# Performance work log

Measured on AMD Instinct MI355X. Metric: run time of the kernel, lower is better.

The kernel has to match this reference:

```python
import jax, jax.numpy as jnp
import numpy as np

B, C, T, L, H = 4, 512, 8, 512, 8


def _normalize(a, eps=1e-12):
    # F.normalize: x / max(||x||_2, eps) along last dim
    n = jnp.linalg.norm(a, axis=-1, keepdims=True)
    return a / jnp.maximum(n, eps)


def setup_inputs() -> dict:
    key = jax.random.key(0)
    ks = jax.random.split(key, 8)
    w = lambda k, shp: (jax.random.normal(k, shp, dtype=jnp.float32) * 0.02)
    return {
        "e": jax.random.normal(ks[0], (B, C, T, L), dtype=jnp.float32),
        "x": jax.random.normal(ks[1], (B, C, T, L), dtype=jnp.float32),
        "Wq": w(ks[2], (C, C)), "bq": jnp.zeros((C,), jnp.float32),
        "Wkv": w(ks[3], (2 * C, C)), "bkv": jnp.zeros((2 * C,), jnp.float32),
        "Wm": w(ks[4], (C, C)), "bm": jnp.zeros((C,), jnp.float32),
        "Wg1": w(ks[5], (C, C)), "bg1": jnp.zeros((C,), jnp.float32),
        "Wg2": w(ks[6], (H, C)), "bg2": jnp.zeros((H,), jnp.float32),
    }


def reference(e, x, Wq, bq, Wkv, bkv, Wm, bm, Wg1, bg1, Wg2, bg2):
    shortcut = x
    xp = jnp.transpose(x, (0, 2, 3, 1))  # (b,t,l,c)
    ep = jnp.transpose(e, (0, 2, 3, 1))  # (b,t,l,c)
    b, t, l, c = xp.shape
    hd = c // H

    # per-(b,t) head gating from pooled e (gate_weights1 == gate_weights in source)
    pooled = ep.mean(axis=2)  # (b,t,c)
    glog = jnp.tanh(pooled @ Wg1.T + bg1) @ Wg2.T + bg2  # (b,t,H)
    gw = jax.nn.softmax(glog, axis=-1)[..., None, None]  # (b,t,H,1,1)

    q = (ep @ Wq.T + bq).reshape(b, t, l, H, hd).transpose(0, 1, 3, 2, 4)  # (b,t,H,l,hd)
    q = _normalize(q)
    kv = (xp @ Wkv.T + bkv).reshape(b, t, l, 2 * H, hd).transpose(0, 1, 3, 2, 4)
    k, v = kv[:, :, :H], kv[:, :, H:]
    k = _normalize(k)
    v = _normalize(v) * gw  # pre-softmax value gating

    scale = jnp.float32(1.0 / np.sqrt(hd))
    att = jax.nn.softmax(jnp.einsum('bthid,bthjd->bthij', q, k) * scale, axis=-1)
    o = jnp.einsum('bthij,bthjd->bthid', att, v) * gw  # post-attention gating

    o = o.transpose(0, 1, 3, 2, 4).reshape(b, t, l, c)
    o = o @ Wm.T + bm
    return jnp.transpose(o, (0, 3, 1, 2)) + shortcut
```

## Files before the change

### kernel.cpp

```cpp
#include <hip/hip_runtime.h>
#include <math.h>

#define B_ 4
#define C_ 512
#define T_ 8
#define L_ 512
#define H_ 8
#define HD_ 64

typedef unsigned short ushort_t;
using short8 = __attribute__((ext_vector_type(8))) short;
using f4 = __attribute__((ext_vector_type(4))) float;

#define GLOAD_LDS(gp, lp)                                                      \
  __builtin_amdgcn_global_load_lds(                                            \
      (const __attribute__((address_space(1))) unsigned int*)(gp),             \
      (__attribute__((address_space(3))) unsigned int*)(lp), 16, 0, 0)

__device__ __forceinline__ unsigned pack_bf16(float a, float b) {
  union { float f; unsigned u; } ua, ub;
  ua.f = a; ub.f = b;
  unsigned ra = (ua.u + 0x7FFFu + ((ua.u >> 16) & 1u)) >> 16;
  unsigned rb = (ub.u + 0x7FFFu + ((ub.u >> 16) & 1u)) >> 16;
  return (rb << 16) | (ra & 0xFFFFu);
}
__device__ __forceinline__ ushort_t bf16_1(float a) {
  union { float f; unsigned u; } ua; ua.f = a;
  return (ushort_t)((ua.u + 0x7FFFu + ((ua.u >> 16) & 1u)) >> 16);
}


__global__ __launch_bounds__(256) void pool_kernel(const float* __restrict__ e,
                                                   float* __restrict__ pooled) {
  int wave = threadIdx.x >> 6;
  int lane = threadIdx.x & 63;
  int r = blockIdx.x * 4 + wave;
  int t = r % T_;
  int c = (r / T_) % C_;
  int b = r / (T_ * C_);
  const float* row = e + (size_t)r * L_;
  float s = 0.f;
#pragma unroll
  for (int i = 0; i < L_ / 64; ++i) s += row[lane + i * 64];
#pragma unroll
  for (int off = 32; off > 0; off >>= 1) s += __shfl_down(s, off, 64);
  if (lane == 0) pooled[(b * T_ + t) * C_ + c] = s * (1.0f / L_);
}

__global__ __launch_bounds__(256) void gate1_kernel(const float* __restrict__ pooled,
                                                    const float* __restrict__ Wg1,
                                                    const float* __restrict__ bg1,
                                                    float* __restrict__ h1) {
  int w = threadIdx.x >> 6, lane = threadIdx.x & 63;
  int row = blockIdx.x * 4 + w;
  int bt = blockIdx.y;
  const float* wr = Wg1 + (size_t)row * C_;
  const float* pr = pooled + bt * C_;
  float s = 0.f;
#pragma unroll
  for (int i = 0; i < 8; ++i) s += wr[lane + i * 64] * pr[lane + i * 64];
#pragma unroll
  for (int off = 32; off > 0; off >>= 1) s += __shfl_down(s, off, 64);
  if (lane == 0) h1[bt * C_ + row] = tanhf(s + bg1[row]);
}

__global__ __launch_bounds__(256) void gate2_kernel(const float* __restrict__ h1,
                                                    const float* __restrict__ Wg2,
                                                    const float* __restrict__ bg2,
                                                    float* __restrict__ gwp) {
  __shared__ float part[256];
  __shared__ float gl[H_];
  int bt = blockIdx.x, tid = threadIdx.x;
  int h = tid >> 5, s = tid & 31;
  const float* w2 = Wg2 + (size_t)h * C_;
  const float* hb = h1 + bt * C_;
  float p = 0.f;
  for (int c = s; c < C_; c += 32) p += w2[c] * hb[c];
  part[tid] = p;
  __syncthreads();
  if (tid < H_) {
    float a = bg2[tid];
    for (int i = 0; i < 32; ++i) a += part[tid * 32 + i];
    gl[tid] = a;
  }
  __syncthreads();
  if (tid == 0) {
    float m = -1e30f;
    for (int i = 0; i < H_; ++i) m = fmaxf(m, gl[i]);
    float sum = 0.f;
    float ex[H_];
    for (int i = 0; i < H_; ++i) { ex[i] = expf(gl[i] - m); sum += ex[i]; }
    for (int i = 0; i < H_; ++i) gwp[bt * H_ + i] = ex[i] / sum;
  }
}

__global__ __launch_bounds__(256) void cvt_kernel(const float* __restrict__ s,
                                                  ushort_t* __restrict__ d) {
  int i = (blockIdx.x * 256 + threadIdx.x) * 8;
  float4 a = *(const float4*)(s + i);
  float4 b = *(const float4*)(s + i + 4);
  uint4 o;
  o.x = pack_bf16(a.x, a.y); o.y = pack_bf16(a.z, a.w);
  o.z = pack_bf16(b.x, b.y); o.w = pack_bf16(b.z, b.w);
  *(uint4*)(d + i) = o;
}

__global__ __launch_bounds__(256) void tconv_kernel(const float* __restrict__ src,
                                                    ushort_t* __restrict__ dst) {
  __shared__ float tb[64][65];
  int tid = threadIdx.x;
  int b = blockIdx.z >> 3, t = blockIdx.z & 7;
  int c0 = blockIdx.y * 64, l0 = blockIdx.x * 64;
  const float* sp = src + (((size_t)(b * C_ + c0) * T_) + t) * L_ + l0;
  int j = tid & 63, i0 = tid >> 6;
#pragma unroll
  for (int p = 0; p < 16; ++p) {
    int i = p * 4 + i0;
    tb[i][j] = sp[(size_t)i * (T_ * L_) + j];
  }
  __syncthreads();
  int ii = (tid & 31) * 2, jj0 = tid >> 5;
  ushort_t* dp = dst + ((size_t)blockIdx.z * L_ + l0) * C_ + c0;
#pragma unroll
  for (int p = 0; p < 8; ++p) {
    int jj = p * 8 + jj0;
    *(unsigned*)(dp + (size_t)jj * C_ + ii) = pack_bf16(tb[ii][jj], tb[ii + 1][jj]);
  }
}

__global__ __launch_bounds__(256, 2) void gemm_mfma(
    const ushort_t* __restrict__ A, const ushort_t* __restrict__ BT,
    const float* __restrict__ bias, int mode,
    float* __restrict__ Out, const float* __restrict__ resid,
    ushort_t* __restrict__ Kdst, ushort_t* __restrict__ Vdst,
    const float* __restrict__ gwp, float qscale) {
  __shared__ alignas(16) ushort_t As[128 * 32];
  __shared__ alignas(16) ushort_t Bs[128 * 32];
  int tid = threadIdx.x;
  int w = tid >> 6, lane = tid & 63, l15 = lane & 15, q = lane >> 4;
  int n0 = blockIdx.x * 128, m0 = blockIdx.y * 128, bt = blockIdx.z;
  int wm = (w >> 1) * 64, wn = (w & 1) * 64;
  const ushort_t* Bbt = BT + (size_t)bt * C_ * C_;

  int c0 = w * 64 + lane, c1 = 256 + w * 64 + lane;
  const ushort_t* ag0 = A + (size_t)(m0 + (c0 >> 2)) * 512 + (c0 & 3) * 8;
  const ushort_t* ag1 = A + (size_t)(m0 + (c1 >> 2)) * 512 + (c1 & 3) * 8;
  const ushort_t* bg0 = Bbt + (size_t)(n0 + (c0 >> 2)) * 512 + (c0 & 3) * 8;
  const ushort_t* bg1 = Bbt + (size_t)(n0 + (c1 >> 2)) * 512 + (c1 & 3) * 8;
  ushort_t* la0 = As + (size_t)(w * 64) * 8;
  ushort_t* la1 = As + (size_t)(256 + w * 64) * 8;
  ushort_t* lb0 = Bs + (size_t)(w * 64) * 8;
  ushort_t* lb1 = Bs + (size_t)(256 + w * 64) * 8;

  f4 acc[4][4];
#pragma unroll
  for (int i = 0; i < 4; ++i)
#pragma unroll
    for (int j = 0; j < 4; ++j) acc[i][j] = (f4){0.f, 0.f, 0.f, 0.f};

  for (int k0 = 0; k0 < 512; k0 += 32) {
    __syncthreads();
    GLOAD_LDS(ag0 + k0, la0);
    GLOAD_LDS(ag1 + k0, la1);
    GLOAD_LDS(bg0 + k0, lb0);
    GLOAD_LDS(bg1 + k0, lb1);
    __syncthreads();
    short8 af[4], bf[4];
#pragma unroll
    for (int mt = 0; mt < 4; ++mt)
      af[mt] = *(const short8*)&As[(size_t)(wm + mt * 16 + l15) * 32 + q * 8];
#pragma unroll
    for (int nt = 0; nt < 4; ++nt)
      bf[nt] = *(const short8*)&Bs[(size_t)(wn + nt * 16 + l15) * 32 + q * 8];
#pragma unroll
    for (int mt = 0; mt < 4; ++mt)
#pragma unroll
      for (int nt = 0; nt < 4; ++nt)
        acc[mt][nt] =
            __builtin_amdgcn_mfma_f32_16x16x32_bf16(af[mt], bf[nt], acc[mt][nt], 0, 0, 0);
  }

#pragma unroll
  for (int mt = 0; mt < 4; ++mt)
#pragma unroll
    for (int r = 0; r < 4; ++r) {
      float bb = bias[m0 + wm + mt * 16 + q * 4 + r];
#pragma unroll
      for (int nt = 0; nt < 4; ++nt) acc[mt][nt][r] += bb;
    }

  if (mode == 0) {
    int b = bt >> 3, t = bt & 7;
    float* Ob = Out + (size_t)b * (C_ * T_ * L_) + (size_t)t * L_;
    const float* Rb = resid + (size_t)b * (C_ * T_ * L_) + (size_t)t * L_;
#pragma unroll
    for (int mt = 0; mt < 4; ++mt)
#pragma unroll
      for (int r = 0; r < 4; ++r) {
        size_t ro = (size_t)(m0 + wm + mt * 16 + q * 4 + r) * (T_ * L_);
#pragma unroll
        for (int nt = 0; nt < 4; ++nt) {
          int n = n0 + wn + nt * 16 + l15;
          Ob[ro + n] = acc[mt][nt][r] + Rb[ro + n];
        }
      }
    return;
  }

  float scale[4];
#pragma unroll
  for (int nt = 0; nt < 4; ++nt) {
    float s = 0.f;
#pragma unroll
    for (int mt = 0; mt < 4; ++mt)
#pragma unroll
      for (int r = 0; r < 4; ++r) s += acc[mt][nt][r] * acc[mt][nt][r];
    s += __shfl_xor(s, 16);
    s += __shfl_xor(s, 32);
    scale[nt] = s;
  }
  int hh = ((m0 + wm) >> 6) & 7;
  bool isv = (mode == 2) && (m0 + wm >= 512);
  float mult = isv ? gwp[bt * H_ + hh] : qscale;
#pragma unroll
  for (int nt = 0; nt < 4; ++nt)
    scale[nt] = mult / fmaxf(sqrtf(scale[nt]), 1e-12f);

  if (!isv) {
    ushort_t* Kb = Kdst + (size_t)(bt * H_ + hh) * 512 * 64;
#pragma unroll
    for (int nt = 0; nt < 4; ++nt) {
      int l = n0 + wn + nt * 16 + l15;
      ushort_t* rowp = Kb + (size_t)l * 64;
#pragma unroll
      for (int mt = 0; mt < 4; ++mt) {
        uint2 pk;
        pk.x = pack_bf16(acc[mt][nt][0] * scale[nt], acc[mt][nt][1] * scale[nt]);
        pk.y = pack_bf16(acc[mt][nt][2] * scale[nt], acc[mt][nt][3] * scale[nt]);
        *(uint2*)&rowp[mt * 16 + q * 4] = pk;
      }
    }
  } else {
    ushort_t* Vb = Vdst + (size_t)(bt * H_ + hh) * 64 * 512;
#pragma unroll
    for (int mt = 0; mt < 4; ++mt)
#pragma unroll
      for (int r = 0; r < 4; ++r) {
        int d = mt * 16 + q * 4 + r;
        ushort_t* rp = Vb + (size_t)d * 512 + n0 + wn;
#pragma unroll
        for (int nt = 0; nt < 4; ++nt)
          rp[nt * 16 + l15] = bf16_1(acc[mt][nt][r] * scale[nt]);
      }
  }
}

__global__ __launch_bounds__(256) void attn_kernel(
    const ushort_t* __restrict__ Qbf, const ushort_t* __restrict__ Kbf,
    const ushort_t* __restrict__ Vbf, const float* __restrict__ gwp,
    ushort_t* __restrict__ obfT) {
  __shared__ alignas(16) ushort_t Ka[64 * 64];
  __shared__ alignas(16) ushort_t Va[64 * 64];

  int tid = threadIdx.x;
  int w = tid >> 6, lane = tid & 63, l15 = lane & 15, q = lane >> 4;
  int i0 = blockIdx.x * 64, h = blockIdx.y, bt = blockIdx.z;
  int iglob = i0 + w * 16 + l15;

  const ushort_t* qrow = Qbf + ((size_t)(bt * H_ + h) * 512 + iglob) * 64;
  short8 qfrag0 = *(const short8*)&qrow[q * 8];
  short8 qfrag1 = *(const short8*)&qrow[32 + q * 8];

  const ushort_t* Kg = Kbf + (size_t)(bt * H_ + h) * 512 * 64;
  const ushort_t* Vg = Vbf + (size_t)(bt * H_ + h) * 64 * 512;

  int cA = w * 64 + lane, cB = 256 + w * 64 + lane;
  const ushort_t* kg0 = Kg + (size_t)(cA >> 3) * 64 + ((cA & 7) ^ ((cA >> 3) & 7)) * 8;
  const ushort_t* kg1 = Kg + (size_t)(cB >> 3) * 64 + ((cB & 7) ^ ((cB >> 3) & 7)) * 8;
  const ushort_t* vg0 = Vg + (size_t)(cA >> 3) * 512 + ((cA & 7) ^ ((cA >> 3) & 7)) * 8;
  const ushort_t* vg1 = Vg + (size_t)(cB >> 3) * 512 + ((cB & 7) ^ ((cB >> 3) & 7)) * 8;
  ushort_t* lk0 = Ka + (size_t)(w * 64) * 8;
  ushort_t* lk1 = Ka + (size_t)(256 + w * 64) * 8;
  ushort_t* lv0 = Va + (size_t)(w * 64) * 8;
  ushort_t* lv1 = Va + (size_t)(256 + w * 64) * 8;

  f4 acc[4];
#pragma unroll
  for (int dt = 0; dt < 4; ++dt) acc[dt] = (f4){0.f, 0.f, 0.f, 0.f};
  float mrun = -3.0e38f, lrun = 0.f;
  bool hi_half = (lane >= 32);
  int qh2 = (q & 1) * 2;

  for (int j0 = 0; j0 < 512; j0 += 64) {
    __syncthreads();
    GLOAD_LDS(kg0 + (size_t)j0 * 64, lk0);
    GLOAD_LDS(kg1 + (size_t)j0 * 64, lk1);
    GLOAD_LDS(vg0 + j0, lv0);
    GLOAD_LDS(vg1 + j0, lv1);
    __syncthreads();

    f4 sc[4];
#pragma unroll
    for (int jt = 0; jt < 4; ++jt) {
      int row = jt * 16 + l15;
      int swz = row & 7;
      short8 k0 = *(const short8*)&Ka[row * 64 + ((q ^ swz) * 8)];
      short8 k1 = *(const short8*)&Ka[row * 64 + (((4 + q) ^ swz) * 8)];
      f4 c = {0.f, 0.f, 0.f, 0.f};
      c = __builtin_amdgcn_mfma_f32_16x16x32_bf16(k0, qfrag0, c, 0, 0, 0);
      c = __builtin_amdgcn_mfma_f32_16x16x32_bf16(k1, qfrag1, c, 0, 0, 0);
      sc[jt] = c;
    }

    float tm = -3.0e38f;
#pragma unroll
    for (int jt = 0; jt < 4; ++jt)
#pragma unroll
      for (int r = 0; r < 4; ++r) tm = fmaxf(tm, sc[jt][r]);
    tm = fmaxf(tm, __shfl_xor(tm, 16));
    tm = fmaxf(tm, __shfl_xor(tm, 32));
    float mn = fmaxf(mrun, tm);
    float alpha = __expf(mrun - mn);
    mrun = mn;
    float ls = 0.f;
#pragma unroll
    for (int jt = 0; jt < 4; ++jt)
#pragma unroll
      for (int r = 0; r < 4; ++r) {
        float p = __expf(sc[jt][r] - mn);
        sc[jt][r] = p;
        ls += p;
      }
    ls += __shfl_xor(ls, 16);
    ls += __shfl_xor(ls, 32);
    lrun = lrun * alpha + ls;
#pragma unroll
    for (int dt = 0; dt < 4; ++dt) acc[dt] = acc[dt] * alpha;

    unsigned pk01[4], pk23[4];
#pragma unroll
    for (int jt = 0; jt < 4; ++jt) {
      pk01[jt] = pack_bf16(sc[jt][0], sc[jt][1]);
      pk23[jt] = pack_bf16(sc[jt][2], sc[jt][3]);
    }

#pragma unroll
    for (int ks2 = 0; ks2 < 2; ++ks2) {
      union { unsigned u[4]; short8 s; } bu;
#pragma unroll
      for (int r = 0; r < 4; ++r) {
        int src = (qh2 + (r >> 1)) * 16 + l15;
        unsigned pl = (r & 1) ? pk23[ks2 * 2] : pk01[ks2 * 2];
        unsigned ph = (r & 1) ? pk23[ks2 * 2 + 1] : pk01[ks2 * 2 + 1];
        unsigned lo = __shfl(pl, src);
        unsigned hi = __shfl(ph, src);
        bu.u[r] = hi_half ? hi : lo;
      }
      short8 bfrag = bu.s;
#pragma unroll
      for (int dt = 0; dt < 4; ++dt) {
        int row = dt * 16 + l15;
        short8 vf =
            *(const short8*)&Va[row * 64 + (((ks2 * 4 + q) ^ (row & 7)) * 8)];
        acc[dt] = __builtin_amdgcn_mfma_f32_16x16x32_bf16(vf, bfrag, acc[dt], 0, 0, 0);
      }
    }
  }

  float g = gwp[bt * H_ + h];
  float inv = g / lrun;
  ushort_t* ob = obfT + ((size_t)(bt * 512 + iglob)) * 512 + h * 64;
#pragma unroll
  for (int dt = 0; dt < 4; ++dt) {
    uint2 pk;
    pk.x = pack_bf16(acc[dt][0] * inv, acc[dt][1] * inv);
    pk.y = pack_bf16(acc[dt][2] * inv, acc[dt][3] * inv);
    *(uint2*)&ob[dt * 16 + q * 4] = pk;
  }
}

extern "C" void kernel_launch(void* const* d_in, const int* in_sizes, int n_in,
                              void* d_out, int out_size, void* d_ws, size_t ws_size,
                              hipStream_t stream) {
  const float* e   = (const float*)d_in[0];
  const float* x   = (const float*)d_in[1];
  const float* Wq  = (const float*)d_in[2];
  const float* bq  = (const float*)d_in[3];
  const float* Wkv = (const float*)d_in[4];
  const float* bkv = (const float*)d_in[5];
  const float* Wm  = (const float*)d_in[6];
  const float* bm  = (const float*)d_in[7];
  const float* Wg1 = (const float*)d_in[8];
  const float* bg1 = (const float*)d_in[9];
  const float* Wg2 = (const float*)d_in[10];
  const float* bg2 = (const float*)d_in[11];
  float* out = (float*)d_out;

  float* ws = (float*)d_ws;
  float* pooled = ws;
  float* gwp    = ws + 16384;
  float* h1buf  = ws + 16640;
  float* fb     = ws + 33024;
  ushort_t* ebfT = (ushort_t*)(fb);
  ushort_t* xbfT = (ushort_t*)(fb + 1 * 4194304);
  ushort_t* Qbf  = (ushort_t*)(fb + 2 * 4194304);
  ushort_t* Kbf  = (ushort_t*)(fb + 3 * 4194304);
  ushort_t* Vbf  = (ushort_t*)(fb + 4 * 4194304);
  ushort_t* obfT = (ushort_t*)(fb + 5 * 4194304);
  ushort_t* Wqb  = (ushort_t*)(fb + 6 * 4194304);
  ushort_t* Wkvb = Wqb + 262144;
  ushort_t* Wmb  = Wkvb + 524288;

  cvt_kernel<<<dim3(128), dim3(256), 0, stream>>>(Wq, Wqb);
  cvt_kernel<<<dim3(256), dim3(256), 0, stream>>>(Wkv, Wkvb);
  cvt_kernel<<<dim3(128), dim3(256), 0, stream>>>(Wm, Wmb);
  tconv_kernel<<<dim3(8, 8, 32), dim3(256), 0, stream>>>(e, ebfT);
  tconv_kernel<<<dim3(8, 8, 32), dim3(256), 0, stream>>>(x, xbfT);
  pool_kernel<<<dim3(B_ * C_ * T_ / 4), dim3(256), 0, stream>>>(e, pooled);
  gate1_kernel<<<dim3(128, 32), dim3(256), 0, stream>>>(pooled, Wg1, bg1, h1buf);
  gate2_kernel<<<dim3(32), dim3(256), 0, stream>>>(h1buf, Wg2, bg2, gwp);
  gemm_mfma<<<dim3(4, 4, 32), dim3(256), 0, stream>>>(
      Wqb, ebfT, bq, 1, nullptr, nullptr, Qbf, nullptr, gwp, 0.125f);
  gemm_mfma<<<dim3(4, 8, 32), dim3(256), 0, stream>>>(
      Wkvb, xbfT, bkv, 2, nullptr, nullptr, Kbf, Vbf, gwp, 1.0f);
  attn_kernel<<<dim3(8, H_, 32), dim3(256), 0, stream>>>(Qbf, Kbf, Vbf, gwp, obfT);
  gemm_mfma<<<dim3(4, 4, 32), dim3(256), 0, stream>>>(
      Wmb, obfT, bm, 0, out, x, nullptr, nullptr, gwp, 1.0f);
}
```

Before: 274.7 us.

## Fuse pooling into transpose-convert and drop online softmax max in attention

The mean-pool over L is folded into the e transpose/convert kernel through atomic adds, which removes a separate full pass over e. The attention kernel is restructured so that one 512-thread block handles all 512 queries of a (bt,h) pair. Each wave holds four query fragments and reads K/V fragments straight from global memory, with no LDS staging or barriers. The running-max rescaling is dropped on the grounds that q and k are unit-normalized, so the scaled scores are bounded and exp cannot overflow. This removes the max reduction and accumulator rescale, but it relies on that normalization bound and increases register pressure.

```diff
diff --git a/kernel.cpp b/kernel.cpp
--- a/kernel.cpp
+++ b/kernel.cpp
@@ -29,23 +29,6 @@
   return (ushort_t)((ua.u + 0x7FFFu + ((ua.u >> 16) & 1u)) >> 16);
 }
 
-
-__global__ __launch_bounds__(256) void pool_kernel(const float* __restrict__ e,
-                                                   float* __restrict__ pooled) {
-  int wave = threadIdx.x >> 6;
-  int lane = threadIdx.x & 63;
-  int r = blockIdx.x * 4 + wave;
-  int t = r % T_;
-  int c = (r / T_) % C_;
-  int b = r / (T_ * C_);
-  const float* row = e + (size_t)r * L_;
-  float s = 0.f;
-#pragma unroll
-  for (int i = 0; i < L_ / 64; ++i) s += row[lane + i * 64];
-#pragma unroll
-  for (int off = 32; off > 0; off >>= 1) s += __shfl_down(s, off, 64);
-  if (lane == 0) pooled[(b * T_ + t) * C_ + c] = s * (1.0f / L_);
-}
 
 __global__ __launch_bounds__(256) void gate1_kernel(const float* __restrict__ pooled,
                                                     const float* __restrict__ Wg1,
@@ -106,7 +89,8 @@
 }
 
 __global__ __launch_bounds__(256) void tconv_kernel(const float* __restrict__ src,
-                                                    ushort_t* __restrict__ dst) {
+                                                    ushort_t* __restrict__ dst,
+                                                    float* __restrict__ pooled) {
   __shared__ float tb[64][65];
   int tid = threadIdx.x;
   int b = blockIdx.z >> 3, t = blockIdx.z & 7;
@@ -119,6 +103,15 @@
     tb[i][j] = sp[(size_t)i * (T_ * L_) + j];
   }
   __syncthreads();
+  if (pooled) {
+    int c = tid >> 2, part = tid & 3;
+    float s = 0.f;
+#pragma unroll
+    for (int k = 0; k < 16; ++k) s += tb[c][part * 16 + k];
+    s += __shfl_down(s, 1);
+    s += __shfl_down(s, 2);
+    if (part == 0) atomicAdd(&pooled[blockIdx.z * C_ + c0 + c], s * (1.0f / L_));
+  }
   int ii = (tid & 31) * 2, jj0 = tid >> 5;
   ushort_t* dp = dst + ((size_t)blockIdx.z * L_ + l0) * C_ + c0;
 #pragma unroll
@@ -255,127 +248,113 @@
   }
 }
 
-__global__ __launch_bounds__(256) void attn_kernel(
+__global__ __launch_bounds__(512, 2) void attn_kernel(
     const ushort_t* __restrict__ Qbf, const ushort_t* __restrict__ Kbf,
     const ushort_t* __restrict__ Vbf, const float* __restrict__ gwp,
     ushort_t* __restrict__ obfT) {
-  __shared__ alignas(16) ushort_t Ka[64 * 64];
-  __shared__ alignas(16) ushort_t Va[64 * 64];
-
   int tid = threadIdx.x;
   int w = tid >> 6, lane = tid & 63, l15 = lane & 15, q = lane >> 4;
-  int i0 = blockIdx.x * 64, h = blockIdx.y, bt = blockIdx.z;
-  int iglob = i0 + w * 16 + l15;
-
-  const ushort_t* qrow = Qbf + ((size_t)(bt * H_ + h) * 512 + iglob) * 64;
-  short8 qfrag0 = *(const short8*)&qrow[q * 8];
-  short8 qfrag1 = *(const short8*)&qrow[32 + q * 8];
-
+  int h = blockIdx.x, bt = blockIdx.y;
+
+  const ushort_t* Qg = Qbf + (size_t)(bt * H_ + h) * 512 * 64;
   const ushort_t* Kg = Kbf + (size_t)(bt * H_ + h) * 512 * 64;
   const ushort_t* Vg = Vbf + (size_t)(bt * H_ + h) * 64 * 512;
 
-  int cA = w * 64 + lane, cB = 256 + w * 64 + lane;
-  const ushort_t* kg0 = Kg + (size_t)(cA >> 3) * 64 + ((cA & 7) ^ ((cA >> 3) & 7)) * 8;
-  const ushort_t* kg1 = Kg + (size_t)(cB >> 3) * 64 + ((cB & 7) ^ ((cB >> 3) & 7)) * 8;
-  const ushort_t* vg0 = Vg + (size_t)(cA >> 3) * 512 + ((cA & 7) ^ ((cA >> 3) & 7)) * 8;
-  const ushort_t* vg1 = Vg + (size_t)(cB >> 3) * 512 + ((cB & 7) ^ ((cB >> 3) & 7)) * 8;
-  ushort_t* lk0 = Ka + (size_t)(w * 64) * 8;
-  ushort_t* lk1 = Ka + (size_t)(256 + w * 64) * 8;
-  ushort_t* lv0 = Va + (size_t)(w * 64) * 8;
-  ushort_t* lv1 = Va + (size_t)(256 + w * 64) * 8;
-
-  f4 acc[4];
-#pragma unroll
-  for (int dt = 0; dt < 4; ++dt) acc[dt] = (f4){0.f, 0.f, 0.f, 0.f};
-  float mrun = -3.0e38f, lrun = 0.f;
+  short8 qf[4][2];
+#pragma unroll
+  for (int f = 0; f < 4; ++f) {
+    const ushort_t* qrow = Qg + (size_t)(w * 64 + f * 16 + l15) * 64;
+    qf[f][0] = *(const short8*)&qrow[q * 8];
+    qf[f][1] = *(const short8*)&qrow[32 + q * 8];
+  }
+
+  f4 acc[4][4];
+#pragma unroll
+  for (int f = 0; f < 4; ++f)
+#pragma unroll
+    for (int dt = 0; dt < 4; ++dt) acc[f][dt] = (f4){0.f, 0.f, 0.f, 0.f};
+  float lsum[4] = {0.f, 0.f, 0.f, 0.f};
   bool hi_half = (lane >= 32);
   int qh2 = (q & 1) * 2;
 
   for (int j0 = 0; j0 < 512; j0 += 64) {
-    __syncthreads();
-    GLOAD_LDS(kg0 + (size_t)j0 * 64, lk0);
-    GLOAD_LDS(kg1 + (size_t)j0 * 64, lk1);
-    GLOAD_LDS(vg0 + j0, lv0);
-    GLOAD_LDS(vg1 + j0, lv1);
-    __syncthreads();
-
-    f4 sc[4];
+    short8 kf[4][2], vf[2][4];
 #pragma unroll
     for (int jt = 0; jt < 4; ++jt) {
-      int row = jt * 16 + l15;
-      int swz = row & 7;
-      short8 k0 = *(const short8*)&Ka[row * 64 + ((q ^ swz) * 8)];
-      short8 k1 = *(const short8*)&Ka[row * 64 + (((4 + q) ^ swz) * 8)];
-      f4 c = {0.f, 0.f, 0.f, 0.f};
-      c = __builtin_amdgcn_mfma_f32_16x16x32_bf16(k0, qfrag0, c, 0, 0, 0);
-      c = __builtin_amdgcn_mfma_f32_16x16x32_bf16(k1, qfrag1, c, 0, 0, 0);
-      sc[jt] = c;
+      const ushort_t* krow = Kg + (size_t)(j0 + jt * 16 + l15) * 64;
+      kf[jt][0] = *(const short8*)&krow[q * 8];
+      kf[jt][1] = *(const short8*)&krow[32 + q * 8];
     }
-
-    float tm = -3.0e38f;
-#pragma unroll
-    for (int jt = 0; jt < 4; ++jt)
-#pragma unroll
-      for (int r = 0; r < 4; ++r) tm = fmaxf(tm, sc[jt][r]);
-    tm = fmaxf(tm, __shfl_xor(tm, 16));
-    tm = fmaxf(tm, __shfl_xor(tm, 32));
-    float mn = fmaxf(mrun, tm);
-    float alpha = __expf(mrun - mn);
-    mrun = mn;
-    float ls = 0.f;
-#pragma unroll
-    for (int jt = 0; jt < 4; ++jt)
-#pragma unroll
-      for (int r = 0; r < 4; ++r) {
-        float p = __expf(sc[jt][r] - mn);
-        sc[jt][r] = p;
-        ls += p;
-      }
+#pragma unroll
+    for (int ks2 = 0; ks2 < 2; ++ks2)
+#pragma unroll
+      for (int dt = 0; dt < 4; ++dt)
+        vf[ks2][dt] = *(const short8*)(Vg + (size_t)(dt * 16 + l15) * 512 + j0 +
+                                       ks2 * 32 + q * 8);
+
+#pragma unroll
+    for (int f = 0; f < 4; ++f) {
+      f4 sc[4];
+#pragma unroll
+      for (int jt = 0; jt < 4; ++jt) {
+        f4 c = {0.f, 0.f, 0.f, 0.f};
+        c = __builtin_amdgcn_mfma_f32_16x16x32_bf16(kf[jt][0], qf[f][0], c, 0, 0, 0);
+        c = __builtin_amdgcn_mfma_f32_16x16x32_bf16(kf[jt][1], qf[f][1], c, 0, 0, 0);
+        sc[jt] = c;
+      }
+      float ls = 0.f;
+#pragma unroll
+      for (int jt = 0; jt < 4; ++jt)
+#pragma unroll
+        for (int r = 0; r < 4; ++r) {
+          float p = __expf(sc[jt][r]);
+          sc[jt][r] = p;
+          ls += p;
+        }
+      lsum[f] += ls;
+
+      unsigned pk01[4], pk23[4];
+#pragma unroll
+      for (int jt = 0; jt < 4; ++jt) {
+        pk01[jt] = pack_bf16(sc[jt][0], sc[jt][1]);
+        pk23[jt] = pack_bf16(sc[jt][2], sc[jt][3]);
+      }
+#pragma unroll
+      for (int ks2 = 0; ks2 < 2; ++ks2) {
+        union { unsigned u[4]; short8 s; } bu;
+#pragma unroll
+        for (int r = 0; r < 4; ++r) {
+          int src = (qh2 + (r >> 1)) * 16 + l15;
+          unsigned pl = (r & 1) ? pk23[ks2 * 2] : pk01[ks2 * 2];
+          unsigned ph = (r & 1) ? pk23[ks2 * 2 + 1] : pk01[ks2 * 2 + 1];
+          unsigned lo = __shfl(pl, src);
+          unsigned hi = __shfl(ph, src);
+          bu.u[r] = hi_half ? hi : lo;
+        }
+#pragma unroll
+        for (int dt = 0; dt < 4; ++dt)
+          acc[f][dt] = __builtin_amdgcn_mfma_f32_16x16x32_bf16(vf[ks2][dt], bu.s,
+                                                               acc[f][dt], 0, 0, 0);
+      }
+    }
+  }
+
+  float g = gwp[bt * H_ + h];
+#pragma unroll
+  for (int f = 0; f < 4; ++f) {
+    float ls = lsum[f];
     ls += __shfl_xor(ls, 16);
     ls += __shfl_xor(ls, 32);
-    lrun = lrun * alpha + ls;
-#pragma unroll
-    for (int dt = 0; dt < 4; ++dt) acc[dt] = acc[dt] * alpha;
-
-    unsigned pk01[4], pk23[4];
-#pragma unroll
-    for (int jt = 0; jt < 4; ++jt) {
-      pk01[jt] = pack_bf16(sc[jt][0], sc[jt][1]);
-      pk23[jt] = pack_bf16(sc[jt][2], sc[jt][3]);
+    float inv = g / ls;
+    int iglob = w * 64 + f * 16 + l15;
+    ushort_t* ob = obfT + ((size_t)(bt * 512 + iglob)) * 512 + h * 64;
+#pragma unroll
+    for (int dt = 0; dt < 4; ++dt) {
+      uint2 pk;
+      pk.x = pack_bf16(acc[f][dt][0] * inv, acc[f][dt][1] * inv);
+      pk.y = pack_bf16(acc[f][dt][2] * inv, acc[f][dt][3] * inv);
+      *(uint2*)&ob[dt * 16 + q * 4] = pk;
     }
-
-#pragma unroll
-    for (int ks2 = 0; ks2 < 2; ++ks2) {
-      union { unsigned u[4]; short8 s; } bu;
-#pragma unroll
-      for (int r = 0; r < 4; ++r) {
-        int src = (qh2 + (r >> 1)) * 16 + l15;
-        unsigned pl = (r & 1) ? pk23[ks2 * 2] : pk01[ks2 * 2];
-        unsigned ph = (r & 1) ? pk23[ks2 * 2 + 1] : pk01[ks2 * 2 + 1];
-        unsigned lo = __shfl(pl, src);
-        unsigned hi = __shfl(ph, src);
-        bu.u[r] = hi_half ? hi : lo;
-      }
-      short8 bfrag = bu.s;
-#pragma unroll
-      for (int dt = 0; dt < 4; ++dt) {
-        int row = dt * 16 + l15;
-        short8 vf =
-            *(const short8*)&Va[row * 64 + (((ks2 * 4 + q) ^ (row & 7)) * 8)];
-        acc[dt] = __builtin_amdgcn_mfma_f32_16x16x32_bf16(vf, bfrag, acc[dt], 0, 0, 0);
-      }
-    }
-  }
-
-  float g = gwp[bt * H_ + h];
-  float inv = g / lrun;
-  ushort_t* ob = obfT + ((size_t)(bt * 512 + iglob)) * 512 + h * 64;
-#pragma unroll
-  for (int dt = 0; dt < 4; ++dt) {
-    uint2 pk;
-    pk.x = pack_bf16(acc[dt][0] * inv, acc[dt][1] * inv);
-    pk.y = pack_bf16(acc[dt][2] * inv, acc[dt][3] * inv);
-    *(uint2*)&ob[dt * 16 + q * 4] = pk;
   }
 }
 
@@ -411,19 +390,19 @@
   ushort_t* Wkvb = Wqb + 262144;
   ushort_t* Wmb  = Wkvb + 524288;
 
+  hipMemsetAsync(pooled, 0, 16384 * sizeof(float), stream);
   cvt_kernel<<<dim3(128), dim3(256), 0, stream>>>(Wq, Wqb);
   cvt_kernel<<<dim3(256), dim3(256), 0, stream>>>(Wkv, Wkvb);
   cvt_kernel<<<dim3(128), dim3(256), 0, stream>>>(Wm, Wmb);
-  tconv_kernel<<<dim3(8, 8, 32), dim3(256), 0, stream>>>(e, ebfT);
-  tconv_kernel<<<dim3(8, 8, 32), dim3(256), 0, stream>>>(x, xbfT);
-  pool_kernel<<<dim3(B_ * C_ * T_ / 4), dim3(256), 0, stream>>>(e, pooled);
+  tconv_kernel<<<dim3(8, 8, 32), dim3(256), 0, stream>>>(e, ebfT, pooled);
+  tconv_kernel<<<dim3(8, 8, 32), dim3(256), 0, stream>>>(x, xbfT, nullptr);
   gate1_kernel<<<dim3(128, 32), dim3(256), 0, stream>>>(pooled, Wg1, bg1, h1buf);
   gate2_kernel<<<dim3(32), dim3(256), 0, stream>>>(h1buf, Wg2, bg2, gwp);
   gemm_mfma<<<dim3(4, 4, 32), dim3(256), 0, stream>>>(
       Wqb, ebfT, bq, 1, nullptr, nullptr, Qbf, nullptr, gwp, 0.125f);
   gemm_mfma<<<dim3(4, 8, 32), dim3(256), 0, stream>>>(
       Wkvb, xbfT, bkv, 2, nullptr, nullptr, Kbf, Vbf, gwp, 1.0f);
-  attn_kernel<<<dim3(8, H_, 32), dim3(256), 0, stream>>>(Qbf, Kbf, Vbf, gwp, obfT);
+  attn_kernel<<<dim3(H_, 32), dim3(512), 0, stream>>>(Qbf, Kbf, Vbf, gwp, obfT);
   gemm_mfma<<<dim3(4, 4, 32), dim3(256), 0, stream>>>(
       Wmb, obfT, bm, 0, out, x, nullptr, nullptr, gwp, 1.0f);
 }
```

Measured after the change: 260.3 us. -5.2%, faster.
